# Optimization experiments

Measured on AMD Instinct MI355X. Metric: run time of the kernel, lower is better.

Reference implementation:

```python
import jax, jax.numpy as jnp
import numpy as np

EMB = 1024

def setup_inputs() -> dict:
    key = jax.random.key(0)
    ks = jax.random.split(key, 7)
    s = 1.0 / np.sqrt(EMB)
    x = jax.random.normal(ks[0], (4, 2048, EMB), dtype=jnp.float32)
    Wk = jax.random.normal(ks[1], (EMB, EMB), dtype=jnp.float32) * s
    bk = jnp.zeros((EMB,), dtype=jnp.float32)
    Wq = jax.random.normal(ks[2], (EMB, EMB), dtype=jnp.float32) * s
    bq = jnp.zeros((EMB,), dtype=jnp.float32)
    Wv = jax.random.normal(ks[3], (EMB, EMB), dtype=jnp.float32) * s
    bv = jnp.zeros((EMB,), dtype=jnp.float32)
    return {"x": x, "Wk": Wk, "bk": bk, "Wq": Wq, "bq": bq, "Wv": Wv, "bv": bv}

def reference(x, Wk, bk, Wq, bq, Wv, bv):
    # Linear layers: x @ W.T + b (torch nn.Linear convention)
    k = jnp.einsum('bse,fe->bsf', x, Wk) + bk
    q = jnp.einsum('bse,fe->bsf', x, Wq) + bq
    v = jnp.einsum('bse,fe->bsf', x, Wv) + bv
    E = x.shape[-1]
    # NOTE: original computes k @ q^T (not q @ k^T) — reproduce faithfully.
    sim = jnp.einsum('bsd,btd->bst', k, q) / jnp.sqrt(jnp.float32(E))
    S = x.shape[1]
    causal = jnp.tril(jnp.ones((S, S), dtype=bool))  # [S,S]
    sim = jnp.where(causal, sim, -jnp.inf)
    attn = jax.nn.softmax(sim, axis=-1)
    return jnp.einsum('bst,btd->bsd', attn, v)
```

## Files before the change

kernel.cpp:

```cpp
#include <hip/hip_runtime.h>
#include <cstdint>


typedef __attribute__((ext_vector_type(8))) _Float16 f16x8;
typedef __attribute__((ext_vector_type(4))) float f32x4;

__device__ __forceinline__ unsigned short f2h(float x) {
  return __builtin_bit_cast(unsigned short, (_Float16)x);
}
__device__ __forceinline__ float h2f(unsigned short u) {
  return (float)__builtin_bit_cast(_Float16, u);
}

__device__ __forceinline__ void lds_dma16(const void* g, void* l) {
  auto gp = reinterpret_cast<const __attribute__((address_space(1))) void*>(
      reinterpret_cast<uintptr_t>(g));
  auto lp = reinterpret_cast<__attribute__((address_space(3))) void*>(
      reinterpret_cast<uintptr_t>(l));
  __builtin_amdgcn_global_load_lds(gp, lp, 16, 0, 0);
}

__device__ __forceinline__ void gemm128(const unsigned short* __restrict__ Ag,
                                        const unsigned short* __restrict__ Bg,
                                        int lda, int ldb, int nk,
                                        unsigned short* As, unsigned short* Bs,
                                        f32x4 acc[4][4]) {
  const int tid = threadIdx.x;
  const int lane = tid & 63, wave = tid >> 6;
  const int wm = wave >> 1, wn = wave & 1;
  const int sr = lane >> 2;
  const int sc = (lane & 3) * 8;
  const int rr = lane & 15, qq = lane >> 4;

#pragma unroll
  for (int i = 0; i < 4; ++i)
#pragma unroll
    for (int j = 0; j < 4; ++j) {
      f32x4 z = {0.f, 0.f, 0.f, 0.f};
      acc[i][j] = z;
    }

  for (int k0 = 0; k0 < nk; k0 += 32) {
#pragma unroll
    for (int c = 0; c < 2; ++c) {
      int chunk = wave * 2 + c;
      int row = chunk * 16 + sr;
      lds_dma16(Ag + (size_t)row * lda + k0 + sc, As + chunk * 512);
      lds_dma16(Bg + (size_t)row * ldb + k0 + sc, Bs + chunk * 512);
    }
    __syncthreads();

    f16x8 af[4], bf[4];
    const unsigned short* Ar = As + (wm * 64 + rr) * 32 + qq * 8;
    const unsigned short* Br = Bs + (wn * 64 + rr) * 32 + qq * 8;
#pragma unroll
    for (int i = 0; i < 4; ++i) af[i] = *(const f16x8*)(Ar + i * 512);
#pragma unroll
    for (int j = 0; j < 4; ++j) bf[j] = *(const f16x8*)(Br + j * 512);
#pragma unroll
    for (int i = 0; i < 4; ++i)
#pragma unroll
      for (int j = 0; j < 4; ++j)
        acc[i][j] = __builtin_amdgcn_mfma_f32_16x16x32_f16(af[i], bf[j],
                                                           acc[i][j], 0, 0, 0);
    __syncthreads();
  }
}

__global__ void cvt_x_kernel(const float* __restrict__ s,
                             unsigned short* __restrict__ d, int n4) {
  int i = blockIdx.x * blockDim.x + threadIdx.x;
  if (i >= n4) return;
  float4 f = ((const float4*)s)[i];
  ushort4 u;
  u.x = f2h(f.x); u.y = f2h(f.y); u.z = f2h(f.z); u.w = f2h(f.w);
  ((ushort4*)d)[i] = u;
}

__global__ void cvt_w_kernel(const float* __restrict__ w0,
                             const float* __restrict__ w1,
                             const float* __restrict__ w2,
                             unsigned short* __restrict__ d) {
  int z = blockIdx.z;
  const float* s = (z == 0) ? w0 : ((z == 1) ? w1 : w2);
  int i = blockIdx.x * blockDim.x + threadIdx.x;
  float4 f = ((const float4*)s)[i];
  ushort4 u;
  u.x = f2h(f.x); u.y = f2h(f.y); u.z = f2h(f.z); u.w = f2h(f.w);
  ((ushort4*)(d + (size_t)z * 1048576))[i] = u;
}

__global__ __launch_bounds__(256) void qkv_gemm_kernel(
    const unsigned short* __restrict__ xh, const unsigned short* __restrict__ wh,
    const float* __restrict__ bk, const float* __restrict__ bq,
    const float* __restrict__ bv, unsigned short* __restrict__ kh,
    unsigned short* __restrict__ qh, unsigned short* __restrict__ vh) {
  __shared__ unsigned short As[128 * 32], Bs[128 * 32];
  const int z = blockIdx.z;
  const unsigned short* W = wh + (size_t)z * 1048576;
  const float* bias = (z == 0) ? bk : ((z == 1) ? bq : bv);
  unsigned short* dst = (z == 0) ? kh : ((z == 1) ? qh : vh);
  const int tn = blockIdx.x, tm = blockIdx.y;

  f32x4 acc[4][4];
  gemm128(xh + (size_t)tm * 128 * 1024, W + (size_t)tn * 128 * 1024,
          1024, 1024, 1024, As, Bs, acc);

  const int lane = threadIdx.x & 63, wave = threadIdx.x >> 6;
  const int wm = wave >> 1, wn = wave & 1, rr = lane & 15, qq = lane >> 4;
  float bj[4];
#pragma unroll
  for (int j = 0; j < 4; ++j)
    bj[j] = bias[tn * 128 + wn * 64 + j * 16 + rr];
#pragma unroll
  for (int i = 0; i < 4; ++i)
#pragma unroll
    for (int reg = 0; reg < 4; ++reg) {
      int gm = tm * 128 + wm * 64 + i * 16 + qq * 4 + reg;
#pragma unroll
      for (int j = 0; j < 4; ++j) {
        int gc = tn * 128 + wn * 64 + j * 16 + rr;
        dst[(size_t)gm * 1024 + gc] = f2h(acc[i][j][reg] + bj[j]);
      }
    }
}

__global__ void transpose_v_kernel(const unsigned short* __restrict__ v,
                                   unsigned short* __restrict__ vT) {
  __shared__ unsigned short tile[32][33];
  const int b = blockIdx.z;
  const unsigned short* vp = v + (size_t)b * 2048 * 1024;
  unsigned short* vtp = vT + (size_t)b * 1024 * 2048;
  const int t0 = blockIdx.x * 32, d0 = blockIdx.y * 32;
  const int x = threadIdx.x, y = threadIdx.y;
#pragma unroll
  for (int i = 0; i < 32; i += 8)
    tile[y + i][x] = vp[(size_t)(t0 + y + i) * 1024 + d0 + x];
  __syncthreads();
#pragma unroll
  for (int i = 0; i < 32; i += 8)
    vtp[(size_t)(d0 + y + i) * 2048 + t0 + x] = tile[x][y + i];
}

__global__ __launch_bounds__(256) void scores_kernel(
    const unsigned short* __restrict__ kh, const unsigned short* __restrict__ qh,
    unsigned short* __restrict__ P) {
  const int tt = blockIdx.x, ts = blockIdx.y, b = blockIdx.z;
  if (tt > ts) return;
  __shared__ unsigned short As[128 * 32], Bs[128 * 32];

  f32x4 acc[4][4];
  gemm128(kh + ((size_t)(b * 2048 + ts * 128)) * 1024,
          qh + ((size_t)(b * 2048 + tt * 128)) * 1024,
          1024, 1024, 1024, As, Bs, acc);

  const int lane = threadIdx.x & 63, wave = threadIdx.x >> 6;
  const int wm = wave >> 1, wn = wave & 1, rr = lane & 15, qq = lane >> 4;
  unsigned short* Pb = P + (size_t)b * 2048 * 2048;
#pragma unroll
  for (int i = 0; i < 4; ++i)
#pragma unroll
    for (int reg = 0; reg < 4; ++reg) {
      int srow = ts * 128 + wm * 64 + i * 16 + qq * 4 + reg;
#pragma unroll
      for (int j = 0; j < 4; ++j) {
        int tcol = tt * 128 + wn * 64 + j * 16 + rr;
        float e = (tcol <= srow) ? __expf(acc[i][j][reg] * 0.03125f - 4.0f)
                                 : 0.0f;
        Pb[(size_t)srow * 2048 + tcol] = f2h(e);
      }
    }
}

__global__ __launch_bounds__(256) void rowsum_kernel(
    const unsigned short* __restrict__ P, float* __restrict__ rinv) {
  const int row = blockIdx.x * 4 + (threadIdx.x >> 6);
  const int lane = threadIdx.x & 63;
  const int s = row & 2047;
  const int len = ((s >> 7) + 1) * 128;
  const unsigned short* Pr = P + (size_t)row * 2048;
  float sum = 0.f;
  for (int t = lane * 8; t < len; t += 512) {
    uint4 u = *(const uint4*)(Pr + t);
    sum += h2f((unsigned short)(u.x & 0xffff)) + h2f((unsigned short)(u.x >> 16));
    sum += h2f((unsigned short)(u.y & 0xffff)) + h2f((unsigned short)(u.y >> 16));
    sum += h2f((unsigned short)(u.z & 0xffff)) + h2f((unsigned short)(u.z >> 16));
    sum += h2f((unsigned short)(u.w & 0xffff)) + h2f((unsigned short)(u.w >> 16));
  }
#pragma unroll
  for (int off = 32; off; off >>= 1) sum += __shfl_xor(sum, off, 64);
  if (lane == 0) rinv[row] = 1.0f / sum;
}

__global__ __launch_bounds__(256) void pv_gemm_kernel(
    const unsigned short* __restrict__ P, const unsigned short* __restrict__ vT,
    const float* __restrict__ rinv, float* __restrict__ out) {
  const int td = blockIdx.x, ts = 15 - blockIdx.y, b = blockIdx.z;
  __shared__ unsigned short As[128 * 32], Bs[128 * 32];

  f32x4 acc[4][4];
  gemm128(P + ((size_t)(b * 2048 + ts * 128)) * 2048,
          vT + ((size_t)(b * 1024 + td * 128)) * 2048,
          2048, 2048, (ts + 1) * 128, As, Bs, acc);

  const int lane = threadIdx.x & 63, wave = threadIdx.x >> 6;
  const int wm = wave >> 1, wn = wave & 1, rr = lane & 15, qq = lane >> 4;
#pragma unroll
  for (int i = 0; i < 4; ++i)
#pragma unroll
    for (int reg = 0; reg < 4; ++reg) {
      int srow = ts * 128 + wm * 64 + i * 16 + qq * 4 + reg;
      float rv = rinv[b * 2048 + srow];
#pragma unroll
      for (int j = 0; j < 4; ++j) {
        int dcol = td * 128 + wn * 64 + j * 16 + rr;
        out[((size_t)(b * 2048 + srow)) * 1024 + dcol] = acc[i][j][reg] * rv;
      }
    }
}

extern "C" void kernel_launch(void* const* d_in, const int* in_sizes, int n_in,
                              void* d_out, int out_size, void* d_ws,
                              size_t ws_size, hipStream_t stream) {
  const float* x  = (const float*)d_in[0];
  const float* Wk = (const float*)d_in[1];
  const float* bk = (const float*)d_in[2];
  const float* Wq = (const float*)d_in[3];
  const float* bq = (const float*)d_in[4];
  const float* Wv = (const float*)d_in[5];
  const float* bv = (const float*)d_in[6];
  float* out = (float*)d_out;

  char* ws = (char*)d_ws;
  const size_t MB = 1ull << 20;
  unsigned short* xh = (unsigned short*)(ws + 0);
  unsigned short* wh = (unsigned short*)(ws + 16 * MB);
  unsigned short* vh = (unsigned short*)(ws + 22 * MB);
  unsigned short* P  = (unsigned short*)(ws + 0);
  unsigned short* kh = (unsigned short*)(ws + 38 * MB);
  unsigned short* qh = (unsigned short*)(ws + 54 * MB);
  unsigned short* vT = (unsigned short*)(ws + 70 * MB);
  float* rinv = (float*)(ws + 86 * MB);

  cvt_x_kernel<<<8192, 256, 0, stream>>>(x, xh, 8388608 / 4);
  cvt_w_kernel<<<dim3(1024, 1, 3), 256, 0, stream>>>(Wk, Wq, Wv, wh);
  qkv_gemm_kernel<<<dim3(8, 64, 3), 256, 0, stream>>>(xh, wh, bk, bq, bv,
                                                      kh, qh, vh);
  transpose_v_kernel<<<dim3(64, 32, 4), dim3(32, 8), 0, stream>>>(vh, vT);
  scores_kernel<<<dim3(16, 16, 4), 256, 0, stream>>>(kh, qh, P);
  rowsum_kernel<<<2048, 256, 0, stream>>>(P, rinv);
  pv_gemm_kernel<<<dim3(8, 16, 4), 256, 0, stream>>>(P, vT, rinv, out);
}
```

Before: 287.6 us.

## Swizzle LDS tiles, fuse conversions, fold row sums into scores kernel

Applies an XOR swizzle to the LDS tile layout used by the shared 128x128 GEMM so the MFMA fragment reads avoid bank conflicts. Merges the x and weight fp16 conversion kernels into one launch and flattens the QKV grid so the three projections share one grid dimension. Removes the separate row-sum kernel by having the scores epilogue reduce each row's exponentials across lanes and atomically add them into a zeroed buffer, with the PV kernel taking a hardware reciprocal. This cuts two launches and one full re-read of P, but adds a memset, float atomics with nondeterministic summation order, and an approximate reciprocal.

```diff
diff --git a/kernel.cpp b/kernel.cpp
--- a/kernel.cpp
+++ b/kernel.cpp
@@ -7,9 +7,6 @@
 
 __device__ __forceinline__ unsigned short f2h(float x) {
   return __builtin_bit_cast(unsigned short, (_Float16)x);
-}
-__device__ __forceinline__ float h2f(unsigned short u) {
-  return (float)__builtin_bit_cast(_Float16, u);
 }
 
 __device__ __forceinline__ void lds_dma16(const void* g, void* l) {
@@ -29,8 +26,9 @@
   const int lane = tid & 63, wave = tid >> 6;
   const int wm = wave >> 1, wn = wave & 1;
   const int sr = lane >> 2;
-  const int sc = (lane & 3) * 8;
+  const int scb = (((lane & 3) ^ ((lane >> 3) & 3)) * 8);
   const int rr = lane & 15, qq = lane >> 4;
+  const int slot = ((qq ^ ((rr >> 1) & 3)) * 8);
 
 #pragma unroll
   for (int i = 0; i < 4; ++i)
@@ -45,14 +43,14 @@
     for (int c = 0; c < 2; ++c) {
       int chunk = wave * 2 + c;
       int row = chunk * 16 + sr;
-      lds_dma16(Ag + (size_t)row * lda + k0 + sc, As + chunk * 512);
-      lds_dma16(Bg + (size_t)row * ldb + k0 + sc, Bs + chunk * 512);
+      lds_dma16(Ag + (size_t)row * lda + k0 + scb, As + chunk * 512);
+      lds_dma16(Bg + (size_t)row * ldb + k0 + scb, Bs + chunk * 512);
     }
     __syncthreads();
 
     f16x8 af[4], bf[4];
-    const unsigned short* Ar = As + (wm * 64 + rr) * 32 + qq * 8;
-    const unsigned short* Br = Bs + (wn * 64 + rr) * 32 + qq * 8;
+    const unsigned short* Ar = As + (wm * 64 + rr) * 32 + slot;
+    const unsigned short* Br = Bs + (wn * 64 + rr) * 32 + slot;
 #pragma unroll
     for (int i = 0; i < 4; ++i) af[i] = *(const f16x8*)(Ar + i * 512);
 #pragma unroll
@@ -67,27 +65,26 @@
   }
 }
 
-__global__ void cvt_x_kernel(const float* __restrict__ s,
-                             unsigned short* __restrict__ d, int n4) {
-  int i = blockIdx.x * blockDim.x + threadIdx.x;
-  if (i >= n4) return;
-  float4 f = ((const float4*)s)[i];
+__global__ void cvt_kernel(const float* __restrict__ x,
+                           const float* __restrict__ w0,
+                           const float* __restrict__ w1,
+                           const float* __restrict__ w2,
+                           unsigned short* __restrict__ dst) {
+  int i = blockIdx.x * 256 + threadIdx.x;
+  const float* s;
+  size_t si;
+  if (i < 2097152) {
+    s = x; si = i;
+  } else {
+    int j = i - 2097152;
+    int z = j >> 18;
+    s = (z == 0) ? w0 : ((z == 1) ? w1 : w2);
+    si = j & 262143;
+  }
+  float4 f = ((const float4*)s)[si];
   ushort4 u;
   u.x = f2h(f.x); u.y = f2h(f.y); u.z = f2h(f.z); u.w = f2h(f.w);
-  ((ushort4*)d)[i] = u;
-}
-
-__global__ void cvt_w_kernel(const float* __restrict__ w0,
-                             const float* __restrict__ w1,
-                             const float* __restrict__ w2,
-                             unsigned short* __restrict__ d) {
-  int z = blockIdx.z;
-  const float* s = (z == 0) ? w0 : ((z == 1) ? w1 : w2);
-  int i = blockIdx.x * blockDim.x + threadIdx.x;
-  float4 f = ((const float4*)s)[i];
-  ushort4 u;
-  u.x = f2h(f.x); u.y = f2h(f.y); u.z = f2h(f.z); u.w = f2h(f.w);
-  ((ushort4*)(d + (size_t)z * 1048576))[i] = u;
+  ((ushort4*)dst)[i] = u;
 }
 
 __global__ __launch_bounds__(256) void qkv_gemm_kernel(
@@ -96,11 +93,11 @@
     const float* __restrict__ bv, unsigned short* __restrict__ kh,
     unsigned short* __restrict__ qh, unsigned short* __restrict__ vh) {
   __shared__ unsigned short As[128 * 32], Bs[128 * 32];
-  const int z = blockIdx.z;
+  const int tn = blockIdx.x & 7, z = blockIdx.x >> 3;
   const unsigned short* W = wh + (size_t)z * 1048576;
   const float* bias = (z == 0) ? bk : ((z == 1) ? bq : bv);
   unsigned short* dst = (z == 0) ? kh : ((z == 1) ? qh : vh);
-  const int tn = blockIdx.x, tm = blockIdx.y;
+  const int tm = blockIdx.y;
 
   f32x4 acc[4][4];
   gemm128(xh + (size_t)tm * 128 * 1024, W + (size_t)tn * 128 * 1024,
@@ -144,7 +141,7 @@
 
 __global__ __launch_bounds__(256) void scores_kernel(
     const unsigned short* __restrict__ kh, const unsigned short* __restrict__ qh,
-    unsigned short* __restrict__ P) {
+    unsigned short* __restrict__ P, float* __restrict__ rsum) {
   const int tt = blockIdx.x, ts = blockIdx.y, b = blockIdx.z;
   if (tt > ts) return;
   __shared__ unsigned short As[128 * 32], Bs[128 * 32];
@@ -157,44 +154,30 @@
   const int lane = threadIdx.x & 63, wave = threadIdx.x >> 6;
   const int wm = wave >> 1, wn = wave & 1, rr = lane & 15, qq = lane >> 4;
   unsigned short* Pb = P + (size_t)b * 2048 * 2048;
+  float* rs = rsum + b * 2048;
 #pragma unroll
   for (int i = 0; i < 4; ++i)
 #pragma unroll
     for (int reg = 0; reg < 4; ++reg) {
       int srow = ts * 128 + wm * 64 + i * 16 + qq * 4 + reg;
+      float p = 0.f;
 #pragma unroll
       for (int j = 0; j < 4; ++j) {
         int tcol = tt * 128 + wn * 64 + j * 16 + rr;
         float e = (tcol <= srow) ? __expf(acc[i][j][reg] * 0.03125f - 4.0f)
                                  : 0.0f;
         Pb[(size_t)srow * 2048 + tcol] = f2h(e);
+        p += e;
       }
-    }
-}
-
-__global__ __launch_bounds__(256) void rowsum_kernel(
-    const unsigned short* __restrict__ P, float* __restrict__ rinv) {
-  const int row = blockIdx.x * 4 + (threadIdx.x >> 6);
-  const int lane = threadIdx.x & 63;
-  const int s = row & 2047;
-  const int len = ((s >> 7) + 1) * 128;
-  const unsigned short* Pr = P + (size_t)row * 2048;
-  float sum = 0.f;
-  for (int t = lane * 8; t < len; t += 512) {
-    uint4 u = *(const uint4*)(Pr + t);
-    sum += h2f((unsigned short)(u.x & 0xffff)) + h2f((unsigned short)(u.x >> 16));
-    sum += h2f((unsigned short)(u.y & 0xffff)) + h2f((unsigned short)(u.y >> 16));
-    sum += h2f((unsigned short)(u.z & 0xffff)) + h2f((unsigned short)(u.z >> 16));
-    sum += h2f((unsigned short)(u.w & 0xffff)) + h2f((unsigned short)(u.w >> 16));
-  }
-#pragma unroll
-  for (int off = 32; off; off >>= 1) sum += __shfl_xor(sum, off, 64);
-  if (lane == 0) rinv[row] = 1.0f / sum;
+#pragma unroll
+      for (int off = 1; off < 16; off <<= 1) p += __shfl_xor(p, off);
+      if (rr == 0) atomicAdd(rs + srow, p);
+    }
 }
 
 __global__ __launch_bounds__(256) void pv_gemm_kernel(
     const unsigned short* __restrict__ P, const unsigned short* __restrict__ vT,
-    const float* __restrict__ rinv, float* __restrict__ out) {
+    const float* __restrict__ rsum, float* __restrict__ out) {
   const int td = blockIdx.x, ts = 15 - blockIdx.y, b = blockIdx.z;
   __shared__ unsigned short As[128 * 32], Bs[128 * 32];
 
@@ -210,7 +193,7 @@
 #pragma unroll
     for (int reg = 0; reg < 4; ++reg) {
       int srow = ts * 128 + wm * 64 + i * 16 + qq * 4 + reg;
-      float rv = rinv[b * 2048 + srow];
+      float rv = __builtin_amdgcn_rcpf(rsum[b * 2048 + srow]);
 #pragma unroll
       for (int j = 0; j < 4; ++j) {
         int dcol = td * 128 + wn * 64 + j * 16 + rr;
@@ -240,14 +223,13 @@
   unsigned short* kh = (unsigned short*)(ws + 38 * MB);
   unsigned short* qh = (unsigned short*)(ws + 54 * MB);
   unsigned short* vT = (unsigned short*)(ws + 70 * MB);
-  float* rinv = (float*)(ws + 86 * MB);
-
-  cvt_x_kernel<<<8192, 256, 0, stream>>>(x, xh, 8388608 / 4);
-  cvt_w_kernel<<<dim3(1024, 1, 3), 256, 0, stream>>>(Wk, Wq, Wv, wh);
-  qkv_gemm_kernel<<<dim3(8, 64, 3), 256, 0, stream>>>(xh, wh, bk, bq, bv,
-                                                      kh, qh, vh);
+  float* rsum = (float*)(ws + 86 * MB);
+
+  hipMemsetAsync(rsum, 0, 8192 * sizeof(float), stream);
+  cvt_kernel<<<11264, 256, 0, stream>>>(x, Wk, Wq, Wv, xh);
+  qkv_gemm_kernel<<<dim3(24, 64), 256, 0, stream>>>(xh, wh, bk, bq, bv,
+                                                    kh, qh, vh);
   transpose_v_kernel<<<dim3(64, 32, 4), dim3(32, 8), 0, stream>>>(vh, vT);
-  scores_kernel<<<dim3(16, 16, 4), 256, 0, stream>>>(kh, qh, P);
-  rowsum_kernel<<<2048, 256, 0, stream>>>(P, rinv);
-  pv_gemm_kernel<<<dim3(8, 16, 4), 256, 0, stream>>>(P, vT, rinv, out);
-}
+  scores_kernel<<<dim3(16, 16, 4), 256, 0, stream>>>(kh, qh, P, rsum);
+  pv_gemm_kernel<<<dim3(8, 16, 4), 256, 0, stream>>>(P, vT, rsum, out);
+}
```

Result: faster. 277.2 us (-3.6%).
